# Optimization experiments

Hardware: AMD Instinct MI355X
Metric: run time of the kernel (lower is better)

Reference implementation:

```python
import jax, jax.numpy as jnp
import numpy as np

N_NODES = 100000
N_EDGES = 1600000
N_GRAPHS = 128
IN_FEATS = 128
H2 = 128
N_CLASSES = 64


def setup_inputs() -> dict:
    key = jax.random.key(0)
    ks = jax.random.split(key, 12)
    return {
        "feat1": jax.random.normal(ks[0], (N_NODES, IN_FEATS), jnp.float32),
        "feat2": jax.random.normal(ks[1], (N_NODES, IN_FEATS), jnp.float32),
        "src1": jax.random.randint(ks[2], (N_EDGES,), 0, N_NODES),
        "dst1": jax.random.randint(ks[3], (N_EDGES,), 0, N_NODES),
        "gid1": jnp.sort(jax.random.randint(ks[4], (N_NODES,), 0, N_GRAPHS)),
        "src2": jax.random.randint(ks[5], (N_EDGES,), 0, N_NODES),
        "dst2": jax.random.randint(ks[6], (N_EDGES,), 0, N_NODES),
        "gid2": jnp.sort(jax.random.randint(ks[7], (N_NODES,), 0, N_GRAPHS)),
        "W": jax.random.normal(ks[8], (IN_FEATS, H2), jnp.float32) * 0.05,
        "b": jax.random.normal(ks[9], (H2,), jnp.float32) * 0.05,
        "Wc": jax.random.normal(ks[10], (H2, N_CLASSES), jnp.float32) * 0.05,
        "bc": jax.random.normal(ks[11], (N_CLASSES,), jnp.float32) * 0.05,
    }


def _gcn_branch(feat, src, dst, gid, W, b, Wc, bc):
    n = feat.shape[0]
    ones = jnp.ones(src.shape[0], feat.dtype)
    # DGL GraphConv norm='both': D_out^{-1/2} on src side, D_in^{-1/2} on dst side
    deg_out = jnp.clip(jax.ops.segment_sum(ones, src, num_segments=n), 1.0)
    deg_in = jnp.clip(jax.ops.segment_sum(ones, dst, num_segments=n), 1.0)
    h = feat * (deg_out ** -0.5)[:, None]
    h = h @ W  # project before aggregation (same linear math, fewer edge FLOPs)
    agg = jax.ops.segment_sum(h[src], dst, num_segments=n)  # [N, H2]
    h = agg * (deg_in ** -0.5)[:, None] + b
    # F.normalize (L2, dim=1, eps=1e-12) -> sigmoid -> relu (identity after sigmoid)
    h = h / jnp.clip(jnp.linalg.norm(h, axis=1, keepdims=True), 1e-12)
    h = jax.nn.relu(jax.nn.sigmoid(h))
    # dropout(0.3) omitted for deterministic reference (identity)
    # mean_nodes per graph
    hg = jax.ops.segment_sum(h, gid, num_segments=N_GRAPHS)
    cnt = jnp.clip(jax.ops.segment_sum(jnp.ones(n, h.dtype), gid, num_segments=N_GRAPHS), 1.0)
    hg = hg / cnt[:, None]
    return hg @ Wc + bc  # [G, C]


def reference(feat1, feat2, src1, dst1, gid1, src2, dst2, gid2, W, b, Wc, bc):
    h1 = _gcn_branch(feat1, src1, dst1, gid1, W, b, Wc, bc)
    h2 = _gcn_branch(feat2, src2, dst2, gid2, W, b, Wc, bc)
    # torch F.pairwise_distance: ||x1 - x2 + eps||_2 with eps=1e-6
    return jnp.linalg.norm(h1 - h2 + 1e-6, axis=1)
```

## Files before the change

### kernel.cpp

```cpp
#include <hip/hip_runtime.h>
#include <hip/hip_fp16.h>
#include <math.h>

#define F 128
#define C 64
#define G 128
#define KMAX 512
#define P1CH 2048
#define CAPB 4608

typedef _Float16 f16x8 __attribute__((ext_vector_type(8)));
typedef float f32x4 __attribute__((ext_vector_type(4)));

__device__ __forceinline__ void atomicAddF(float* p, float v) {
  __hip_atomic_fetch_add(p, v, __ATOMIC_RELAXED, __HIP_MEMORY_SCOPE_AGENT);
}

__global__ __launch_bounds__(256) void fscale_kernel(
    const float* __restrict__ feat1, const float* __restrict__ feat2,
    const float* __restrict__ dno1, const float* __restrict__ dno2,
    unsigned char* __restrict__ fs1, unsigned char* __restrict__ fs2, int N) {
  const float* feat = blockIdx.y ? feat2 : feat1;
  const float* dno = blockIdx.y ? dno2 : dno1;
  unsigned char* fs = blockIdx.y ? fs2 : fs1;
  int i = blockIdx.x * blockDim.x + threadIdx.x;
  if (i >= N * (F / 8)) return;
  int node = i >> 4;
  float dn = dno[node];
  float4 v0 = ((const float4*)feat)[i * 2];
  float4 v1 = ((const float4*)feat)[i * 2 + 1];
  int w0 = __builtin_amdgcn_cvt_pk_fp8_f32(v0.x * dn, v0.y * dn, 0, false);
  w0 = __builtin_amdgcn_cvt_pk_fp8_f32(v0.z * dn, v0.w * dn, w0, true);
  int w1 = __builtin_amdgcn_cvt_pk_fp8_f32(v1.x * dn, v1.y * dn, 0, false);
  w1 = __builtin_amdgcn_cvt_pk_fp8_f32(v1.z * dn, v1.w * dn, w1, true);
  uint2 pk;
  pk.x = (unsigned)w0;
  pk.y = (unsigned)w1;
  ((uint2*)fs)[i] = pk;
}

__global__ __launch_bounds__(256) void wconv_kernel(const float* __restrict__ Wg,
                                                    _Float16* __restrict__ Wt) {
  int tid = threadIdx.x;
#pragma unroll
  for (int i = 0; i < 8; ++i) {
    int f = tid + i * 256;
    int lane = f & 63;
    int ks = (f >> 6) & 3;
    int t = f >> 8;
    int n = t * 16 + (lane & 15);
    int k0 = ks * 32 + ((lane >> 4) << 3);
    f16x8 v;
#pragma unroll
    for (int j = 0; j < 8; ++j) v[j] = (_Float16)Wg[(k0 + j) * F + n];
    ((f16x8*)Wt)[f] = v;
  }
}

__global__ __launch_bounds__(128) void cnt_kernel(const int* __restrict__ gid1,
                                                  const int* __restrict__ gid2,
                                                  int* __restrict__ cnt1,
                                                  int* __restrict__ cnt2, int N) {
  const int* gid = blockIdx.x ? gid2 : gid1;
  int* cnt = blockIdx.x ? cnt2 : cnt1;
  int g = threadIdx.x;
  int lo = 0, hi = N;
  while (lo < hi) { int m = (lo + hi) >> 1; if (gid[m] < g) lo = m + 1; else hi = m; }
  int lo2 = lo, hi2 = N;
  while (lo2 < hi2) { int m = (lo2 + hi2) >> 1; if (gid[m] <= g) lo2 = m + 1; else hi2 = m; }
  cnt[g] = lo2 - lo;
}

__global__ __launch_bounds__(256) void pass1_kernel(
    const int* __restrict__ src1, const int* __restrict__ dst1,
    const int* __restrict__ src2, const int* __restrict__ dst2,
    int* __restrict__ bcntD1, int* __restrict__ bcntD2,
    int* __restrict__ bcntS1, int* __restrict__ bcntS2,
    unsigned* __restrict__ epkD1, unsigned* __restrict__ epkD2,
    unsigned char* __restrict__ epkS81, unsigned char* __restrict__ epkS82,
    int E, int K) {
  const int* src = blockIdx.y ? src2 : src1;
  const int* dst = blockIdx.y ? dst2 : dst1;
  int* bcntD = blockIdx.y ? bcntD2 : bcntD1;
  int* bcntS = blockIdx.y ? bcntS2 : bcntS1;
  unsigned* epkD = blockIdx.y ? epkD2 : epkD1;
  unsigned char* epkS8 = blockIdx.y ? epkS82 : epkS81;

  __shared__ int cntD[KMAX], resD[KMAX], baseD[KMAX], curD[KMAX];
  __shared__ int cntS[KMAX], resS[KMAX], baseS[KMAX], curS[KMAX];
  __shared__ unsigned stageD[P1CH];
  __shared__ unsigned char stageS[P1CH];
  __shared__ unsigned short bkD[P1CH];
  __shared__ unsigned short bkS[P1CH];

  int t = threadIdx.x;
  int lane = t & 63;
  int wv = t >> 6;

  for (int k = t; k < K; k += 256) { cntD[k] = 0; cntS[k] = 0; }
  __syncthreads();

  int e0 = blockIdx.x * P1CH;
  int e1 = e0 + P1CH; if (e1 > E) e1 = E;
  int M = e1 - e0;
  for (int i = e0 + t; i < e1; i += 256) {
    atomicAdd(&cntD[dst[i] >> 8], 1);
    atomicAdd(&cntS[src[i] >> 8], 1);
  }
  __syncthreads();

  if (wv == 0) {
    int carry = 0;
    for (int b0 = 0; b0 < K; b0 += 64) {
      int k = b0 + lane;
      int v = (k < K) ? cntD[k] : 0;
      int x = v;
#pragma unroll
      for (int off = 1; off < 64; off <<= 1) {
        int y = __shfl_up(x, off);
        if (lane >= off) x += y;
      }
      if (k < K) baseD[k] = carry + x - v;
      carry += __shfl(x, 63);
    }
  } else if (wv == 1) {
    int carry = 0;
    for (int b0 = 0; b0 < K; b0 += 64) {
      int k = b0 + lane;
      int v = (k < K) ? cntS[k] : 0;
      int x = v;
#pragma unroll
      for (int off = 1; off < 64; off <<= 1) {
        int y = __shfl_up(x, off);
        if (lane >= off) x += y;
      }
      if (k < K) baseS[k] = carry + x - v;
      carry += __shfl(x, 63);
    }
  }
  __syncthreads();

  for (int k = t; k < K; k += 256) {
    int c = cntD[k];
    resD[k] = c ? atomicAdd(&bcntD[k], c) : 0;
    int c2 = cntS[k];
    resS[k] = c2 ? atomicAdd(&bcntS[k], c2) : 0;
    curD[k] = baseD[k];
    curS[k] = baseS[k];
  }
  __syncthreads();

  for (int i = e0 + t; i < e1; i += 256) {
    int d = dst[i];
    int s = src[i];
    int kd = d >> 8;
    int p = atomicAdd(&curD[kd], 1);
    stageD[p] = ((unsigned)(d & 255) << 24) | (unsigned)s;
    bkD[p] = (unsigned short)kd;
    int ks = s >> 8;
    int q = atomicAdd(&curS[ks], 1);
    stageS[q] = (unsigned char)(s & 255);
    bkS[q] = (unsigned short)ks;
  }
  __syncthreads();

  for (int i = t; i < M; i += 256) {
    int bk = bkD[i];
    unsigned pos = (unsigned)(resD[bk] + (i - baseD[bk]));
    if (pos < CAPB) epkD[(size_t)bk * CAPB + pos] = stageD[i];
  }
  for (int i = t; i < M; i += 256) {
    int bk = bkS[i];
    unsigned pos = (unsigned)(resS[bk] + (i - baseS[bk]));
    if (pos < CAPB) epkS8[(size_t)bk * CAPB + pos] = stageS[i];
  }
}

__global__ __launch_bounds__(256) void pass2_kernel(
    const int* __restrict__ bcntD1, const int* __restrict__ bcntD2,
    unsigned* __restrict__ epk1, unsigned* __restrict__ epk2,
    int* __restrict__ degi1, int* __restrict__ degi2,
    int* __restrict__ cursor1, int* __restrict__ cursor2, int N) {
  const int* bcntD = blockIdx.y ? bcntD2 : bcntD1;
  unsigned* epk = blockIdx.y ? epk2 : epk1;
  int* degi = blockIdx.y ? degi2 : degi1;
  int* cursor = blockIdx.y ? cursor2 : cursor1;

  __shared__ unsigned pk[CAPB];
  __shared__ int lcnt[256];
  __shared__ int lcur[256];

  int b = blockIdx.x;
  int t = threadIdx.x;
  int s0 = b * CAPB;
  int M = bcntD[b]; if (M > CAPB) M = CAPB;

  lcnt[t] = 0;
  for (int e = t; e < M; e += 256) pk[e] = epk[s0 + e];
  __syncthreads();
  for (int e = t; e < M; e += 256) atomicAdd(&lcnt[pk[e] >> 24], 1);
  __syncthreads();

  int v = lcnt[t];
  lcur[t] = v;
  __syncthreads();
  for (int off = 1; off < 256; off <<= 1) {
    int x = (t >= off) ? lcur[t - off] : 0;
    __syncthreads();
    lcur[t] += x;
    __syncthreads();
  }
  int excl = lcur[t] - v;
  int startp = s0 + excl;
  int node = (b << 8) + t;
  if (node < N) {
    degi[node] = v;
    cursor[node] = startp;
  }
  __syncthreads();
  lcur[t] = startp;
  __syncthreads();
  for (int e = t; e < M; e += 256) {
    unsigned p = pk[e];
    int dl = p >> 24;
    int pos = atomicAdd(&lcur[dl], 1);
    epk[pos] = p & 0xFFFFFFu;
  }
}

__global__ __launch_bounds__(256) void pass2c_kernel(
    const int* __restrict__ bcntS1, const int* __restrict__ bcntS2,
    const unsigned char* __restrict__ epk1, const unsigned char* __restrict__ epk2,
    float* __restrict__ dno1, float* __restrict__ dno2, int N) {
  const int* bcntS = blockIdx.y ? bcntS2 : bcntS1;
  const unsigned char* epk = blockIdx.y ? epk2 : epk1;
  float* dno = blockIdx.y ? dno2 : dno1;

  __shared__ int lcnt[256];
  int b = blockIdx.x;
  int t = threadIdx.x;
  int s0 = b * CAPB;
  int M = bcntS[b]; if (M > CAPB) M = CAPB;
  lcnt[t] = 0;
  __syncthreads();
  for (int e = t; e < M; e += 256)
    atomicAdd(&lcnt[epk[s0 + e]], 1);
  __syncthreads();
  int node = (b << 8) + t;
  if (node < N) {
    int a = lcnt[t]; if (a < 1) a = 1;
    dno[node] = 1.0f / sqrtf((float)a);
  }
}

#define ACCP(rv)                                                        \
  do {                                                                  \
    auto f0 = __builtin_amdgcn_cvt_pk_f32_fp8((int)(rv).x, false);      \
    auto f1 = __builtin_amdgcn_cvt_pk_f32_fp8((int)(rv).x, true);       \
    auto f2 = __builtin_amdgcn_cvt_pk_f32_fp8((int)(rv).y, false);      \
    auto f3 = __builtin_amdgcn_cvt_pk_f32_fp8((int)(rv).y, true);       \
    a0.x += f0[0]; a0.y += f0[1]; a1.x += f1[0]; a1.y += f1[1];         \
    a2.x += f2[0]; a2.y += f2[1]; a3.x += f3[0]; a3.y += f3[1];         \
  } while (0)

__global__ __launch_bounds__(256) void gather_kernel(
    const int* __restrict__ esrc1, const int* __restrict__ cursor1,
    const int* __restrict__ degi1, const unsigned char* __restrict__ fs1,
    __half* __restrict__ aggh1,
    const int* __restrict__ esrc2, const int* __restrict__ cursor2,
    const int* __restrict__ degi2, const unsigned char* __restrict__ fs2,
    __half* __restrict__ aggh2, int N) {
  const int* esrc = blockIdx.y ? esrc2 : esrc1;
  const int* cursor = blockIdx.y ? cursor2 : cursor1;
  const int* degi = blockIdx.y ? degi2 : degi1;
  const unsigned char* featsc = blockIdx.y ? fs2 : fs1;
  __half* aggh = blockIdx.y ? aggh2 : aggh1;

  int node = blockIdx.x * 16 + (threadIdx.x >> 4);
  int l = threadIdx.x & 15;
  if (node >= N) return;
  int cnt = degi[node];
  int start = cursor[node];
  const unsigned char* fl = featsc + l * 8;

  float2 a0 = {0.f, 0.f}, a1 = {0.f, 0.f}, a2 = {0.f, 0.f}, a3 = {0.f, 0.f};

  for (int j0 = 0; j0 < cnt; j0 += 16) {
    int nb = cnt - j0; if (nb > 16) nb = 16;
    int myi = (l < nb) ? __builtin_nontemporal_load(&esrc[start + j0 + l]) : 0;
    int k = 0;
    for (; k + 8 <= nb; k += 8) {
      int s0 = __shfl(myi, k, 16);
      int s1 = __shfl(myi, k + 1, 16);
      int s2 = __shfl(myi, k + 2, 16);
      int s3 = __shfl(myi, k + 3, 16);
      int s4 = __shfl(myi, k + 4, 16);
      int s5 = __shfl(myi, k + 5, 16);
      int s6 = __shfl(myi, k + 6, 16);
      int s7 = __shfl(myi, k + 7, 16);
      uint2 v0 = *(const uint2*)(fl + (size_t)s0 * F);
      uint2 v1 = *(const uint2*)(fl + (size_t)s1 * F);
      uint2 v2 = *(const uint2*)(fl + (size_t)s2 * F);
      uint2 v3 = *(const uint2*)(fl + (size_t)s3 * F);
      uint2 v4 = *(const uint2*)(fl + (size_t)s4 * F);
      uint2 v5 = *(const uint2*)(fl + (size_t)s5 * F);
      uint2 v6 = *(const uint2*)(fl + (size_t)s6 * F);
      uint2 v7 = *(const uint2*)(fl + (size_t)s7 * F);
      ACCP(v0);
      ACCP(v1);
      ACCP(v2);
      ACCP(v3);
      ACCP(v4);
      ACCP(v5);
      ACCP(v6);
      ACCP(v7);
    }
    for (; k + 4 <= nb; k += 4) {
      int s0 = __shfl(myi, k, 16);
      int s1 = __shfl(myi, k + 1, 16);
      int s2 = __shfl(myi, k + 2, 16);
      int s3 = __shfl(myi, k + 3, 16);
      uint2 v0 = *(const uint2*)(fl + (size_t)s0 * F);
      uint2 v1 = *(const uint2*)(fl + (size_t)s1 * F);
      uint2 v2 = *(const uint2*)(fl + (size_t)s2 * F);
      uint2 v3 = *(const uint2*)(fl + (size_t)s3 * F);
      ACCP(v0);
      ACCP(v1);
      ACCP(v2);
      ACCP(v3);
    }
    for (; k < nb; ++k) {
      int s = __shfl(myi, k, 16);
      uint2 v = *(const uint2*)(fl + (size_t)s * F);
      ACCP(v);
    }
  }

  f16x8 hv;
  hv[0] = (_Float16)a0.x; hv[1] = (_Float16)a0.y;
  hv[2] = (_Float16)a1.x; hv[3] = (_Float16)a1.y;
  hv[4] = (_Float16)a2.x; hv[5] = (_Float16)a2.y;
  hv[6] = (_Float16)a3.x; hv[7] = (_Float16)a3.y;
  __builtin_nontemporal_store(hv, (f16x8*)(aggh + (size_t)node * F) + l);
}

__global__ __launch_bounds__(256) void gemm_epi_kernel(
    const __half* __restrict__ agg1, const int* __restrict__ degi1,
    const int* __restrict__ gid1, float* __restrict__ hg1,
    const __half* __restrict__ agg2, const int* __restrict__ degi2,
    const int* __restrict__ gid2, float* __restrict__ hg2,
    const _Float16* __restrict__ Wt, const float* __restrict__ bg, int N) {
  const __half* agg = blockIdx.y ? agg2 : agg1;
  const int* degi = blockIdx.y ? degi2 : degi1;
  const int* gid = blockIdx.y ? gid2 : gid1;
  float* hg = blockIdx.y ? hg2 : hg1;

  __shared__ __align__(16) _Float16 Wl[16384];
  __shared__ float hred[4][F];
  __shared__ int sgid[4];

  int tid = threadIdx.x;
  int wv = tid >> 6;
  int lane = tid & 63;
  int ln = lane & 15;
  int quad = lane >> 4;

  {
    const f16x8* src = (const f16x8*)Wt;
    f16x8* dst = (f16x8*)Wl;
#pragma unroll
    for (int i = 0; i < 8; ++i) dst[tid + i * 256] = src[tid + i * 256];
  }
  __syncthreads();

  int rbase = (blockIdx.x * 4 + wv) * 16;
  bool wave_active = rbase < N;

  int arow = rbase + ln; if (arow >= N) arow = N - 1;
  const _Float16* arow_p = (const _Float16*)(agg + (size_t)arow * F);
  f16x8 a[4];
#pragma unroll
  for (int ks = 0; ks < 4; ++ks)
    a[ks] = *(const f16x8*)(arow_p + ks * 32 + quad * 8);

  f32x4 acc[8];
#pragma unroll
  for (int t = 0; t < 8; ++t) acc[t] = (f32x4){0.f, 0.f, 0.f, 0.f};

#pragma unroll
  for (int t = 0; t < 8; ++t) {
#pragma unroll
    for (int ks = 0; ks < 4; ++ks) {
      f16x8 b = *(const f16x8*)&Wl[(((t << 2) + ks) * 64 + lane) * 8];
      acc[t] = __builtin_amdgcn_mfma_f32_16x16x32_f16(a[ks], b, acc[t], 0, 0, 0);
    }
  }

  float dnr[4]; int gg[4]; bool valid[4];
#pragma unroll
  for (int r = 0; r < 4; ++r) {
    int row = rbase + quad * 4 + r;
    valid[r] = row < N;
    int rc = valid[r] ? row : (N - 1);
    int dv = degi[rc]; if (dv < 1) dv = 1;
    dnr[r] = 1.0f / sqrtf((float)dv);
    gg[r] = gid[rc];
  }
  float bb[8];
#pragma unroll
  for (int t = 0; t < 8; ++t) bb[t] = bg[t * 16 + ln];

  float y[8][4], ssq[4];
#pragma unroll
  for (int r = 0; r < 4; ++r) ssq[r] = 0.f;
#pragma unroll
  for (int t = 0; t < 8; ++t) {
#pragma unroll
    for (int r = 0; r < 4; ++r) {
      float v = acc[t][r] * dnr[r] + bb[t];
      y[t][r] = v;
      ssq[r] += v * v;
    }
  }
#pragma unroll
  for (int m = 1; m < 16; m <<= 1) {
#pragma unroll
    for (int r = 0; r < 4; ++r) ssq[r] += __shfl_xor(ssq[r], m);
  }
  float u[8][4];
#pragma unroll
  for (int r = 0; r < 4; ++r) {
    float inv = 1.0f / fmaxf(sqrtf(ssq[r]), 1e-12f);
#pragma unroll
    for (int t = 0; t < 8; ++t) {
      float s = 1.0f / (1.0f + expf(-y[t][r] * inv));
      u[t][r] = valid[r] ? s : 0.0f;
    }
  }

  int rlast = rbase + 15; if (rlast >= N) rlast = N - 1;
  bool uniform = wave_active && (rbase + 15 < N) && (gid[rbase] == gid[rlast]);
  if (uniform) {
    float cs[8];
#pragma unroll
    for (int t = 0; t < 8; ++t) {
      cs[t] = u[t][0] + u[t][1] + u[t][2] + u[t][3];
      cs[t] += __shfl_xor(cs[t], 16);
      cs[t] += __shfl_xor(cs[t], 32);
    }
    if (lane == 0) sgid[wv] = gid[rbase];
    if (lane < 16) {
#pragma unroll
      for (int t = 0; t < 8; ++t) hred[wv][t * 16 + lane] = cs[t];
    }
  } else {
    if (lane == 0) sgid[wv] = -1;
    if (wave_active) {
#pragma unroll
      for (int r = 0; r < 4; ++r) {
        if (!valid[r]) continue;
#pragma unroll
        for (int t = 0; t < 8; ++t)
          atomicAddF(&hg[(size_t)gg[r] * F + t * 16 + ln], u[t][r]);
      }
    }
  }
  __syncthreads();
  if (tid < F) {
    int s0 = sgid[0], s1 = sgid[1], s2 = sgid[2], s3 = sgid[3];
    if (s0 >= 0 && s0 == s1 && s0 == s2 && s0 == s3) {
      atomicAddF(&hg[(size_t)s0 * F + tid],
                 hred[0][tid] + hred[1][tid] + hred[2][tid] + hred[3][tid]);
    } else {
      if (s0 >= 0) atomicAddF(&hg[(size_t)s0 * F + tid], hred[0][tid]);
      if (s1 >= 0) atomicAddF(&hg[(size_t)s1 * F + tid], hred[1][tid]);
      if (s2 >= 0) atomicAddF(&hg[(size_t)s2 * F + tid], hred[2][tid]);
      if (s3 >= 0) atomicAddF(&hg[(size_t)s3 * F + tid], hred[3][tid]);
    }
  }
}

__global__ __launch_bounds__(64) void final_kernel(
    const float* __restrict__ hg1, const int* __restrict__ cnt1,
    const float* __restrict__ hg2, const int* __restrict__ cnt2,
    const float* __restrict__ Wc, const float* __restrict__ bc,
    float* __restrict__ out) {
  __shared__ float v1[F], v2[F];
  int g = blockIdx.x, c = threadIdx.x;
  float ic1 = 1.0f / fmaxf((float)cnt1[g], 1.0f);
  float ic2 = 1.0f / fmaxf((float)cnt2[g], 1.0f);
  for (int i = c; i < F; i += 64) {
    v1[i] = hg1[(size_t)g * F + i] * ic1;
    v2[i] = hg2[(size_t)g * F + i] * ic2;
  }
  __syncthreads();
  float z1 = bc[c], z2 = bc[c];
  for (int k = 0; k < F; ++k) {
    float w = Wc[k * C + c];
    z1 += v1[k] * w;
    z2 += v2[k] * w;
  }
  float d = z1 - z2 + 1e-6f;
  d *= d;
#pragma unroll
  for (int m = 1; m < 64; m <<= 1) d += __shfl_xor(d, m);
  if (c == 0) out[g] = sqrtf(d);
}

extern "C" void kernel_launch(void* const* d_in, const int* in_sizes, int n_in,
                              void* d_out, int out_size, void* d_ws, size_t ws_size,
                              hipStream_t stream) {
  const float* feat1 = (const float*)d_in[0];
  const float* feat2 = (const float*)d_in[1];
  const int* src1 = (const int*)d_in[2];
  const int* dst1 = (const int*)d_in[3];
  const int* gid1 = (const int*)d_in[4];
  const int* src2 = (const int*)d_in[5];
  const int* dst2 = (const int*)d_in[6];
  const int* gid2 = (const int*)d_in[7];
  const float* Wg = (const float*)d_in[8];
  const float* bg = (const float*)d_in[9];
  const float* Wc = (const float*)d_in[10];
  const float* bc = (const float*)d_in[11];
  float* out = (float*)d_out;

  int N = in_sizes[0] / F;
  int E = in_sizes[2];
  int K = (N + 255) >> 8;
  if (K > KMAX) return;

  char* w = (char*)d_ws;
  float* hg1 = (float*)w; w += (size_t)G * F * 4;
  float* hg2 = (float*)w; w += (size_t)G * F * 4;
  int* bcntD1 = (int*)w; w += KMAX * 4;
  int* bcntD2 = (int*)w; w += KMAX * 4;
  int* bcntS1 = (int*)w; w += KMAX * 4;
  int* bcntS2 = (int*)w; w += KMAX * 4;
  size_t zbytes = (size_t)(w - (char*)d_ws);
  __half* aggh1 = (__half*)w; w += (size_t)N * F * 2;
  __half* aggh2 = (__half*)w; w += (size_t)N * F * 2;
  unsigned char* fs1 = (unsigned char*)w; w += (size_t)N * F;
  unsigned char* fs2 = (unsigned char*)w; w += (size_t)N * F;
  unsigned* epkD1 = (unsigned*)w; w += (size_t)K * CAPB * 4;
  unsigned* epkD2 = (unsigned*)w; w += (size_t)K * CAPB * 4;
  int* degi1 = (int*)w; w += (size_t)N * 4;
  int* degi2 = (int*)w; w += (size_t)N * 4;
  float* dno1 = (float*)w; w += (size_t)N * 4;
  float* dno2 = (float*)w; w += (size_t)N * 4;
  int* cursor1 = (int*)w; w += (size_t)N * 4;
  int* cursor2 = (int*)w; w += (size_t)N * 4;
  int* cnt1 = (int*)w; w += 128 * 4;
  int* cnt2 = (int*)w; w += 128 * 4;
  _Float16* Wt = (_Float16*)w; w += (size_t)F * F * 2;
  if ((size_t)(w - (char*)d_ws) > ws_size) return;

  unsigned char* epkS81 = (unsigned char*)aggh1;
  unsigned char* epkS82 = epkS81 + (size_t)K * CAPB;

  (void)hipMemsetAsync(d_ws, 0, zbytes, stream);

  wconv_kernel<<<1, 256, 0, stream>>>(Wg, Wt);
  cnt_kernel<<<2, 128, 0, stream>>>(gid1, gid2, cnt1, cnt2, N);

  int p1b = (E + P1CH - 1) / P1CH;
  pass1_kernel<<<dim3(p1b, 2), 256, 0, stream>>>(
      src1, dst1, src2, dst2, bcntD1, bcntD2, bcntS1, bcntS2,
      epkD1, epkD2, epkS81, epkS82, E, K);
  pass2_kernel<<<dim3(K, 2), 256, 0, stream>>>(bcntD1, bcntD2, epkD1, epkD2,
                                               degi1, degi2, cursor1, cursor2, N);
  pass2c_kernel<<<dim3(K, 2), 256, 0, stream>>>(bcntS1, bcntS2, epkS81, epkS82,
                                                dno1, dno2, N);

  int fsb = (N * (F / 8) + 255) / 256;
  fscale_kernel<<<dim3(fsb, 2), 256, 0, stream>>>(feat1, feat2, dno1, dno2, fs1, fs2, N);

  int gbr = (N + 15) / 16;
  gather_kernel<<<dim3(gbr, 2), 256, 0, stream>>>(
      (const int*)epkD1, cursor1, degi1, fs1, aggh1,
      (const int*)epkD2, cursor2, degi2, fs2, aggh2, N);

  int gb = (N + 63) / 64;
  gemm_epi_kernel<<<dim3(gb, 2), 256, 0, stream>>>(
      aggh1, degi1, gid1, hg1, aggh2, degi2, gid2, hg2, Wt, bg, N);

  final_kernel<<<G, 64, 0, stream>>>(hg1, cnt1, hg2, cnt2, Wc, bc, out);
}
```

Measured before the change: 380.5 us.

## Fuse per-bucket edge sort into gather kernel using shared-memory sorted edges

Merges the pass2 local counting sort with the gather kernel: each block loads one 256-node destination bucket, sorts its edges by destination in LDS, and then gathers fp8 source features for its 256 nodes directly from the LDS-sorted list. This removes a kernel launch, the cursor arrays and the global write-back and re-read of the sorted edge list. It also drops the separate cursor shared arrays in pass1 by reusing the base arrays. The cost is lower parallelism: the gather now runs about 391x2 blocks of 256 threads instead of about 6250x2 blocks, and each block uses roughly 37KB of LDS. That may reduce occupancy and the ability to hide latency on the random feature loads.

After: 379.1 us. No clear change (-0.4%).

```diff
diff --git a/kernel.cpp b/kernel.cpp
--- a/kernel.cpp
+++ b/kernel.cpp
@@ -86,8 +86,8 @@
   unsigned* epkD = blockIdx.y ? epkD2 : epkD1;
   unsigned char* epkS8 = blockIdx.y ? epkS82 : epkS81;
 
-  __shared__ int cntD[KMAX], resD[KMAX], baseD[KMAX], curD[KMAX];
-  __shared__ int cntS[KMAX], resS[KMAX], baseS[KMAX], curS[KMAX];
+  __shared__ int cntD[KMAX], resD[KMAX], baseD[KMAX];
+  __shared__ int cntS[KMAX], resS[KMAX], baseS[KMAX];
   __shared__ unsigned stageD[P1CH];
   __shared__ unsigned char stageS[P1CH];
   __shared__ unsigned short bkD[P1CH];
@@ -145,8 +145,6 @@
     resD[k] = c ? atomicAdd(&bcntD[k], c) : 0;
     int c2 = cntS[k];
     resS[k] = c2 ? atomicAdd(&bcntS[k], c2) : 0;
-    curD[k] = baseD[k];
-    curS[k] = baseS[k];
   }
   __syncthreads();
 
@@ -154,11 +152,11 @@
     int d = dst[i];
     int s = src[i];
     int kd = d >> 8;
-    int p = atomicAdd(&curD[kd], 1);
+    int p = atomicAdd(&baseD[kd], 1);
     stageD[p] = ((unsigned)(d & 255) << 24) | (unsigned)s;
     bkD[p] = (unsigned short)kd;
     int ks = s >> 8;
-    int q = atomicAdd(&curS[ks], 1);
+    int q = atomicAdd(&baseS[ks], 1);
     stageS[q] = (unsigned char)(s & 255);
     bkS[q] = (unsigned short)ks;
   }
@@ -166,65 +164,13 @@
 
   for (int i = t; i < M; i += 256) {
     int bk = bkD[i];
-    unsigned pos = (unsigned)(resD[bk] + (i - baseD[bk]));
+    unsigned pos = (unsigned)(resD[bk] + (i - (baseD[bk] - cntD[bk])));
     if (pos < CAPB) epkD[(size_t)bk * CAPB + pos] = stageD[i];
   }
   for (int i = t; i < M; i += 256) {
     int bk = bkS[i];
-    unsigned pos = (unsigned)(resS[bk] + (i - baseS[bk]));
+    unsigned pos = (unsigned)(resS[bk] + (i - (baseS[bk] - cntS[bk])));
     if (pos < CAPB) epkS8[(size_t)bk * CAPB + pos] = stageS[i];
-  }
-}
-
-__global__ __launch_bounds__(256) void pass2_kernel(
-    const int* __restrict__ bcntD1, const int* __restrict__ bcntD2,
-    unsigned* __restrict__ epk1, unsigned* __restrict__ epk2,
-    int* __restrict__ degi1, int* __restrict__ degi2,
-    int* __restrict__ cursor1, int* __restrict__ cursor2, int N) {
-  const int* bcntD = blockIdx.y ? bcntD2 : bcntD1;
-  unsigned* epk = blockIdx.y ? epk2 : epk1;
-  int* degi = blockIdx.y ? degi2 : degi1;
-  int* cursor = blockIdx.y ? cursor2 : cursor1;
-
-  __shared__ unsigned pk[CAPB];
-  __shared__ int lcnt[256];
-  __shared__ int lcur[256];
-
-  int b = blockIdx.x;
-  int t = threadIdx.x;
-  int s0 = b * CAPB;
-  int M = bcntD[b]; if (M > CAPB) M = CAPB;
-
-  lcnt[t] = 0;
-  for (int e = t; e < M; e += 256) pk[e] = epk[s0 + e];
-  __syncthreads();
-  for (int e = t; e < M; e += 256) atomicAdd(&lcnt[pk[e] >> 24], 1);
-  __syncthreads();
-
-  int v = lcnt[t];
-  lcur[t] = v;
-  __syncthreads();
-  for (int off = 1; off < 256; off <<= 1) {
-    int x = (t >= off) ? lcur[t - off] : 0;
-    __syncthreads();
-    lcur[t] += x;
-    __syncthreads();
-  }
-  int excl = lcur[t] - v;
-  int startp = s0 + excl;
-  int node = (b << 8) + t;
-  if (node < N) {
-    degi[node] = v;
-    cursor[node] = startp;
-  }
-  __syncthreads();
-  lcur[t] = startp;
-  __syncthreads();
-  for (int e = t; e < M; e += 256) {
-    unsigned p = pk[e];
-    int dl = p >> 24;
-    int pos = atomicAdd(&lcur[dl], 1);
-    epk[pos] = p & 0xFFFFFFu;
   }
 }
 
@@ -263,85 +209,128 @@
     a2.x += f2[0]; a2.y += f2[1]; a3.x += f3[0]; a3.y += f3[1];         \
   } while (0)
 
-__global__ __launch_bounds__(256) void gather_kernel(
-    const int* __restrict__ esrc1, const int* __restrict__ cursor1,
-    const int* __restrict__ degi1, const unsigned char* __restrict__ fs1,
-    __half* __restrict__ aggh1,
-    const int* __restrict__ esrc2, const int* __restrict__ cursor2,
-    const int* __restrict__ degi2, const unsigned char* __restrict__ fs2,
-    __half* __restrict__ aggh2, int N) {
-  const int* esrc = blockIdx.y ? esrc2 : esrc1;
-  const int* cursor = blockIdx.y ? cursor2 : cursor1;
-  const int* degi = blockIdx.y ? degi2 : degi1;
+__global__ __launch_bounds__(256) void p2g_kernel(
+    const int* __restrict__ bcntD1, const int* __restrict__ bcntD2,
+    const unsigned* __restrict__ epk1, const unsigned* __restrict__ epk2,
+    int* __restrict__ degi1, int* __restrict__ degi2,
+    const unsigned char* __restrict__ fs1, const unsigned char* __restrict__ fs2,
+    __half* __restrict__ aggh1, __half* __restrict__ aggh2, int N) {
+  const int* bcntD = blockIdx.y ? bcntD2 : bcntD1;
+  const unsigned* epk = blockIdx.y ? epk2 : epk1;
+  int* degi = blockIdx.y ? degi2 : degi1;
   const unsigned char* featsc = blockIdx.y ? fs2 : fs1;
   __half* aggh = blockIdx.y ? aggh2 : aggh1;
 
-  int node = blockIdx.x * 16 + (threadIdx.x >> 4);
-  int l = threadIdx.x & 15;
-  if (node >= N) return;
-  int cnt = degi[node];
-  int start = cursor[node];
+  __shared__ unsigned pk[CAPB];
+  __shared__ unsigned srt[CAPB];
+  __shared__ int lcnt[256];
+  __shared__ int lcur[256];
+  __shared__ int scur[256];
+
+  int b = blockIdx.x;
+  int t = threadIdx.x;
+  size_t s0 = (size_t)b * CAPB;
+  int M = bcntD[b]; if (M > CAPB) M = CAPB;
+
+  lcnt[t] = 0;
+  for (int e = t; e < M; e += 256) pk[e] = epk[s0 + e];
+  __syncthreads();
+  for (int e = t; e < M; e += 256) atomicAdd(&lcnt[pk[e] >> 24], 1);
+  __syncthreads();
+
+  int v = lcnt[t];
+  lcur[t] = v;
+  __syncthreads();
+  for (int off = 1; off < 256; off <<= 1) {
+    int x = (t >= off) ? lcur[t - off] : 0;
+    __syncthreads();
+    lcur[t] += x;
+    __syncthreads();
+  }
+  int node = (b << 8) + t;
+  if (node < N) degi[node] = v;
+  scur[t] = lcur[t] - v;
+  __syncthreads();
+
+  for (int e = t; e < M; e += 256) {
+    unsigned p = pk[e];
+    int dl = p >> 24;
+    int pos = atomicAdd(&scur[dl], 1);
+    srt[pos] = p & 0xFFFFFFu;
+  }
+  __syncthreads();
+
+  int g = t >> 4;
+  int l = t & 15;
   const unsigned char* fl = featsc + l * 8;
 
-  float2 a0 = {0.f, 0.f}, a1 = {0.f, 0.f}, a2 = {0.f, 0.f}, a3 = {0.f, 0.f};
-
-  for (int j0 = 0; j0 < cnt; j0 += 16) {
-    int nb = cnt - j0; if (nb > 16) nb = 16;
-    int myi = (l < nb) ? __builtin_nontemporal_load(&esrc[start + j0 + l]) : 0;
-    int k = 0;
-    for (; k + 8 <= nb; k += 8) {
-      int s0 = __shfl(myi, k, 16);
-      int s1 = __shfl(myi, k + 1, 16);
-      int s2 = __shfl(myi, k + 2, 16);
-      int s3 = __shfl(myi, k + 3, 16);
-      int s4 = __shfl(myi, k + 4, 16);
-      int s5 = __shfl(myi, k + 5, 16);
-      int s6 = __shfl(myi, k + 6, 16);
-      int s7 = __shfl(myi, k + 7, 16);
-      uint2 v0 = *(const uint2*)(fl + (size_t)s0 * F);
-      uint2 v1 = *(const uint2*)(fl + (size_t)s1 * F);
-      uint2 v2 = *(const uint2*)(fl + (size_t)s2 * F);
-      uint2 v3 = *(const uint2*)(fl + (size_t)s3 * F);
-      uint2 v4 = *(const uint2*)(fl + (size_t)s4 * F);
-      uint2 v5 = *(const uint2*)(fl + (size_t)s5 * F);
-      uint2 v6 = *(const uint2*)(fl + (size_t)s6 * F);
-      uint2 v7 = *(const uint2*)(fl + (size_t)s7 * F);
-      ACCP(v0);
-      ACCP(v1);
-      ACCP(v2);
-      ACCP(v3);
-      ACCP(v4);
-      ACCP(v5);
-      ACCP(v6);
-      ACCP(v7);
-    }
-    for (; k + 4 <= nb; k += 4) {
-      int s0 = __shfl(myi, k, 16);
-      int s1 = __shfl(myi, k + 1, 16);
-      int s2 = __shfl(myi, k + 2, 16);
-      int s3 = __shfl(myi, k + 3, 16);
-      uint2 v0 = *(const uint2*)(fl + (size_t)s0 * F);
-      uint2 v1 = *(const uint2*)(fl + (size_t)s1 * F);
-      uint2 v2 = *(const uint2*)(fl + (size_t)s2 * F);
-      uint2 v3 = *(const uint2*)(fl + (size_t)s3 * F);
-      ACCP(v0);
-      ACCP(v1);
-      ACCP(v2);
-      ACCP(v3);
-    }
-    for (; k < nb; ++k) {
-      int s = __shfl(myi, k, 16);
-      uint2 v = *(const uint2*)(fl + (size_t)s * F);
-      ACCP(v);
-    }
-  }
-
-  f16x8 hv;
-  hv[0] = (_Float16)a0.x; hv[1] = (_Float16)a0.y;
-  hv[2] = (_Float16)a1.x; hv[3] = (_Float16)a1.y;
-  hv[4] = (_Float16)a2.x; hv[5] = (_Float16)a2.y;
-  hv[6] = (_Float16)a3.x; hv[7] = (_Float16)a3.y;
-  __builtin_nontemporal_store(hv, (f16x8*)(aggh + (size_t)node * F) + l);
+  for (int nn = 0; nn < 16; ++nn) {
+    int n = (g << 4) + nn;
+    int node2 = (b << 8) + n;
+    if (node2 >= N) break;
+    int cnt = lcnt[n];
+    int start = lcur[n] - cnt;
+
+    float2 a0 = {0.f, 0.f}, a1 = {0.f, 0.f}, a2 = {0.f, 0.f}, a3 = {0.f, 0.f};
+
+    for (int j0 = 0; j0 < cnt; j0 += 16) {
+      int nb = cnt - j0; if (nb > 16) nb = 16;
+      int myi = (l < nb) ? (int)srt[start + j0 + l] : 0;
+      int k = 0;
+      for (; k + 8 <= nb; k += 8) {
+        int s0_ = __shfl(myi, k, 16);
+        int s1_ = __shfl(myi, k + 1, 16);
+        int s2_ = __shfl(myi, k + 2, 16);
+        int s3_ = __shfl(myi, k + 3, 16);
+        int s4_ = __shfl(myi, k + 4, 16);
+        int s5_ = __shfl(myi, k + 5, 16);
+        int s6_ = __shfl(myi, k + 6, 16);
+        int s7_ = __shfl(myi, k + 7, 16);
+        uint2 v0 = *(const uint2*)(fl + (size_t)s0_ * F);
+        uint2 v1 = *(const uint2*)(fl + (size_t)s1_ * F);
+        uint2 v2 = *(const uint2*)(fl + (size_t)s2_ * F);
+        uint2 v3 = *(const uint2*)(fl + (size_t)s3_ * F);
+        uint2 v4 = *(const uint2*)(fl + (size_t)s4_ * F);
+        uint2 v5 = *(const uint2*)(fl + (size_t)s5_ * F);
+        uint2 v6 = *(const uint2*)(fl + (size_t)s6_ * F);
+        uint2 v7 = *(const uint2*)(fl + (size_t)s7_ * F);
+        ACCP(v0);
+        ACCP(v1);
+        ACCP(v2);
+        ACCP(v3);
+        ACCP(v4);
+        ACCP(v5);
+        ACCP(v6);
+        ACCP(v7);
+      }
+      for (; k + 4 <= nb; k += 4) {
+        int s0_ = __shfl(myi, k, 16);
+        int s1_ = __shfl(myi, k + 1, 16);
+        int s2_ = __shfl(myi, k + 2, 16);
+        int s3_ = __shfl(myi, k + 3, 16);
+        uint2 v0 = *(const uint2*)(fl + (size_t)s0_ * F);
+        uint2 v1 = *(const uint2*)(fl + (size_t)s1_ * F);
+        uint2 v2 = *(const uint2*)(fl + (size_t)s2_ * F);
+        uint2 v3 = *(const uint2*)(fl + (size_t)s3_ * F);
+        ACCP(v0);
+        ACCP(v1);
+        ACCP(v2);
+        ACCP(v3);
+      }
+      for (; k < nb; ++k) {
+        int s_ = __shfl(myi, k, 16);
+        uint2 vv = *(const uint2*)(fl + (size_t)s_ * F);
+        ACCP(vv);
+      }
+    }
+
+    f16x8 hv;
+    hv[0] = (_Float16)a0.x; hv[1] = (_Float16)a0.y;
+    hv[2] = (_Float16)a1.x; hv[3] = (_Float16)a1.y;
+    hv[4] = (_Float16)a2.x; hv[5] = (_Float16)a2.y;
+    hv[6] = (_Float16)a3.x; hv[7] = (_Float16)a3.y;
+    __builtin_nontemporal_store(hv, (f16x8*)(aggh + (size_t)node2 * F) + l);
+  }
 }
 
 __global__ __launch_bounds__(256) void gemm_epi_kernel(
@@ -547,8 +536,6 @@
   int* degi2 = (int*)w; w += (size_t)N * 4;
   float* dno1 = (float*)w; w += (size_t)N * 4;
   float* dno2 = (float*)w; w += (size_t)N * 4;
-  int* cursor1 = (int*)w; w += (size_t)N * 4;
-  int* cursor2 = (int*)w; w += (size_t)N * 4;
   int* cnt1 = (int*)w; w += 128 * 4;
   int* cnt2 = (int*)w; w += 128 * 4;
   _Float16* Wt = (_Float16*)w; w += (size_t)F * F * 2;
@@ -566,18 +553,14 @@
   pass1_kernel<<<dim3(p1b, 2), 256, 0, stream>>>(
       src1, dst1, src2, dst2, bcntD1, bcntD2, bcntS1, bcntS2,
       epkD1, epkD2, epkS81, epkS82, E, K);
-  pass2_kernel<<<dim3(K, 2), 256, 0, stream>>>(bcntD1, bcntD2, epkD1, epkD2,
-                                               degi1, degi2, cursor1, cursor2, N);
   pass2c_kernel<<<dim3(K, 2), 256, 0, stream>>>(bcntS1, bcntS2, epkS81, epkS82,
                                                 dno1, dno2, N);
 
   int fsb = (N * (F / 8) + 255) / 256;
   fscale_kernel<<<dim3(fsb, 2), 256, 0, stream>>>(feat1, feat2, dno1, dno2, fs1, fs2, N);
 
-  int gbr = (N + 15) / 16;
-  gather_kernel<<<dim3(gbr, 2), 256, 0, stream>>>(
-      (const int*)epkD1, cursor1, degi1, fs1, aggh1,
-      (const int*)epkD2, cursor2, degi2, fs2, aggh2, N);
+  p2g_kernel<<<dim3(K, 2), 256, 0, stream>>>(
+      bcntD1, bcntD2, epkD1, epkD2, degi1, degi2, fs1, fs2, aggh1, aggh2, N);
 
   int gb = (N + 63) / 64;
   gemm_epi_kernel<<<dim3(gb, 2), 256, 0, stream>>>(
```
